# Optimization experiments

Measured on AMD Instinct MI355X. Metric: run time of the kernel, lower is better.

Reference implementation:

```python
import jax, jax.numpy as jnp
import numpy as np

EMBED_DIM = 1024
HEAD_NUM = 16
HEAD_DIM = EMBED_DIM // HEAD_NUM
T, B, S = 2048, 4, 2048


def setup_inputs() -> dict:
    key = jax.random.key(0)
    ks = jax.random.split(key, 11)
    s = 0.02
    return {
        "query": jax.random.normal(ks[0], (T, B, EMBED_DIM), jnp.float32),
        "key": jax.random.normal(ks[1], (S, B, EMBED_DIM), jnp.float32),
        "value": jax.random.normal(ks[2], (S, B, EMBED_DIM), jnp.float32),
        "q_proj_weight": jax.random.normal(ks[3], (EMBED_DIM, EMBED_DIM), jnp.float32) * s,
        "k_proj_weight": jax.random.normal(ks[4], (EMBED_DIM, EMBED_DIM), jnp.float32) * s,
        "v_proj_weight": jax.random.normal(ks[5], (EMBED_DIM, EMBED_DIM), jnp.float32) * s,
        "in_proj_bias": jax.random.normal(ks[6], (3 * EMBED_DIM,), jnp.float32) * s,
        "bias_k": jax.random.normal(ks[7], (1, 1, EMBED_DIM), jnp.float32) * s,
        "bias_v": jax.random.normal(ks[8], (1, 1, EMBED_DIM), jnp.float32) * s,
        "out_proj_weight": jax.random.normal(ks[9], (EMBED_DIM, EMBED_DIM), jnp.float32) * s,
        "out_proj_bias": jax.random.normal(ks[10], (EMBED_DIM,), jnp.float32) * s,
    }


def reference(query, key, value, q_proj_weight, k_proj_weight, v_proj_weight,
              in_proj_bias, bias_k, bias_v, out_proj_weight, out_proj_bias):
    t, b, e = query.shape
    h, hd = HEAD_NUM, HEAD_DIM
    scaling = float(hd) ** -0.5
    # input projections (F.linear: x @ W.T + b)
    q = (query @ q_proj_weight.T + in_proj_bias[:e]) * scaling          # [T,B,E]
    k = key @ k_proj_weight.T + in_proj_bias[e:2 * e]                   # [S,B,E]
    v = value @ v_proj_weight.T + in_proj_bias[2 * e:]                  # [S,B,E]
    # append bias_k / bias_v token along the sequence dim
    k = jnp.concatenate([k, jnp.broadcast_to(bias_k, (1, b, e))], axis=0)  # [S+1,B,E]
    v = jnp.concatenate([v, jnp.broadcast_to(bias_v, (1, b, e))], axis=0)  # [S+1,B,E]
    # split heads: [L, B, E] -> [B*H, L, hd]
    q = q.reshape(t, b * h, hd).transpose(1, 0, 2)
    k = k.reshape(-1, b * h, hd).transpose(1, 0, 2)
    v = v.reshape(-1, b * h, hd).transpose(1, 0, 2)
    # full O(T*S) attention, as in the original bmm->softmax->bmm
    weights = jax.nn.softmax(jnp.einsum('nqd,nkd->nqk', q, k), axis=-1)  # [B*H,T,S+1]
    out = jnp.einsum('nqk,nkd->nqd', weights, v)                         # [B*H,T,hd]
    out = out.transpose(1, 0, 2).reshape(t, b, e)
    out = out @ out_proj_weight.T + out_proj_bias
    avg_weights = weights.sum(axis=1) / h                                # [B*H,S+1]
    return out, avg_weights
```

## Files before the change

### kernel.cpp

```cpp
#include <hip/hip_runtime.h>

#define T_DIM 2048
#define B_DIM 4
#define S_DIM 2048
#define E_DIM 1024
#define H_NUM 16
#define HD    64
#define NH    64
#define SP1   2049
#define SPAD  2112
#define NCHUNK 33
#define NTOKE ((size_t)T_DIM * B_DIM * E_DIM)

typedef short bf16x8 __attribute__((ext_vector_type(8)));
typedef short bf16x4 __attribute__((ext_vector_type(4)));
typedef float f32x4  __attribute__((ext_vector_type(4)));
typedef float f32x16 __attribute__((ext_vector_type(16)));
typedef unsigned int u32;

#define QSCALE 0.18033688011112042f

#if __has_builtin(__builtin_amdgcn_exp2f)
__device__ __forceinline__ float exp2_fast(float x) { return __builtin_amdgcn_exp2f(x); }
#else
__device__ __forceinline__ float exp2_fast(float x) { return __expf(x * 0.6931471805599453f); }
#endif

__device__ __forceinline__ unsigned short f2bf(float x) {
    union { float f; unsigned int u; } v; v.f = x;
    unsigned int r = v.u + 0x7FFFu + ((v.u >> 16) & 1u);
    return (unsigned short)(r >> 16);
}

__device__ __forceinline__ u32 cvtpk_bf16(float lo, float hi) {
    u32 r;
    asm("v_cvt_pk_bf16_f32 %0, %1, %2" : "=v"(r) : "v"(lo), "v"(hi));
    return r;
}
__device__ __forceinline__ void plswap(u32& a, u32& b) {
    asm("v_permlane32_swap_b32 %0, %1" : "+v"(a), "+v"(b));
}

__device__ __forceinline__ void load_lds16(const void* g, void* l) {
    __builtin_amdgcn_global_load_lds(
        (const __attribute__((address_space(1))) unsigned int*)g,
        (__attribute__((address_space(3))) unsigned int*)l, 16, 0, 0);
}

__global__ __launch_bounds__(256)
void cvt_all(const float* __restrict__ q, const float* __restrict__ k,
             const float* __restrict__ v, const float* __restrict__ w0,
             const float* __restrict__ w1, const float* __restrict__ w2,
             const float* __restrict__ w3, short* __restrict__ indst,
             short* __restrict__ wdst, short* __restrict__ k_h,
             short* __restrict__ v_h, const float* __restrict__ bias_k,
             const float* __restrict__ bias_v)
{
    const int y = blockIdx.y;
    if (y < 3) {
        const float* src = (y == 0) ? q : (y == 1) ? k : v;
        short* d = indst + (size_t)y * NTOKE;
        const size_t i = (size_t)blockIdx.x * 256 + threadIdx.x;
        const float4* s = reinterpret_cast<const float4*>(src) + i * 2;
        float4 a = s[0], b = s[1];
        uint4 o;
        o.x = cvtpk_bf16(a.x, a.y); o.y = cvtpk_bf16(a.z, a.w);
        o.z = cvtpk_bf16(b.x, b.y); o.w = cvtpk_bf16(b.z, b.w);
        *(reinterpret_cast<uint4*>(d) + i) = o;
    } else {
        const size_t gi = (size_t)blockIdx.x * 256 + threadIdx.x;
        const size_t per = (size_t)E_DIM * E_DIM / 8;
        if (gi < 4 * per) {
            const int wsel = (int)(gi / per);
            const size_t i = gi % per;
            const float* src = (wsel == 0) ? w0 : (wsel == 1) ? w1 : (wsel == 2) ? w2 : w3;
            short* d = wdst + (size_t)wsel * E_DIM * E_DIM;
            const float4* s = reinterpret_cast<const float4*>(src) + i * 2;
            float4 a = s[0], b = s[1];
            uint4 o;
            o.x = cvtpk_bf16(a.x, a.y); o.y = cvtpk_bf16(a.z, a.w);
            o.z = cvtpk_bf16(b.x, b.y); o.w = cvtpk_bf16(b.z, b.w);
            *(reinterpret_cast<uint4*>(d) + i) = o;
        } else {
            const size_t fi = gi - 4 * per;
            if (fi < (size_t)(SPAD - S_DIM) * NH * HD) {
                const int d   = (int)(fi & 63);
                const int row = (int)((fi >> 6) & 63);
                const int n   = (int)(fi >> 12);
                short bk = 0, bv = 0;
                if (row == 0) {
                    bk = (short)f2bf(bias_k[(n & 15) * HD + d]);
                    bv = (short)f2bf(bias_v[(n & 15) * HD + d]);
                }
                const size_t idx = ((size_t)n * SPAD + S_DIM + row) * HD + d;
                k_h[idx] = bk;
                v_h[idx] = bv;
            }
        }
    }
}

__global__ __launch_bounds__(256, 2)
void gemm_qkv(const short* __restrict__ Abase, const short* __restrict__ Wall,
              const float* __restrict__ biasAll, short* __restrict__ outp)
{
    __shared__ short As[2][128][64];
    __shared__ short Bs[2][128][64];
    const int bm = blockIdx.x, bn = blockIdx.y;
    const int z = blockIdx.z;
    const short* Az = Abase + (size_t)z * NTOKE;
    const short* W  = Wall + (size_t)z * E_DIM * E_DIM;
    const float* bias = biasAll + z * E_DIM;

    const int tid = threadIdx.x;
    const int l = tid & 63, w = tid >> 6;
    const int wr = w >> 1, wc = w & 1;
    const int lr = l & 15, lg = l >> 4;
    const int srow = tid >> 3, scol = (tid & 7) * 8;

    auto stage = [&](int b, int k0) {
#pragma unroll
        for (int r = 0; r < 4; ++r) {
            const int row = r * 32 + srow;
            load_lds16(Az + (size_t)(bm * 128 + row) * E_DIM + k0 + scol, &As[b][row][scol]);
            load_lds16(W + (size_t)(bn * 128 + row) * E_DIM + k0 + scol, &Bs[b][row][scol]);
        }
    };

    stage(0, 0);
    __syncthreads();

    f32x4 acc[4][4] = {};
    int buf = 0;

    for (int k0 = 0; k0 < E_DIM; k0 += 64) {
        if (k0 + 64 < E_DIM) stage(buf ^ 1, k0 + 64);

        __builtin_amdgcn_s_setprio(1);
#pragma unroll
        for (int c = 0; c < 2; ++c) {
            bf16x8 af[4], bf[4];
#pragma unroll
            for (int mi = 0; mi < 4; ++mi)
                af[mi] = *reinterpret_cast<const bf16x8*>(&As[buf][wr * 64 + mi * 16 + lr][c * 32 + lg * 8]);
#pragma unroll
            for (int ni = 0; ni < 4; ++ni)
                bf[ni] = *reinterpret_cast<const bf16x8*>(&Bs[buf][wc * 64 + ni * 16 + lr][c * 32 + lg * 8]);
#pragma unroll
            for (int mi = 0; mi < 4; ++mi)
#pragma unroll
                for (int ni = 0; ni < 4; ++ni)
                    acc[mi][ni] = __builtin_amdgcn_mfma_f32_16x16x32_bf16(
                        af[mi], bf[ni], acc[mi][ni], 0, 0, 0);
        }
        __builtin_amdgcn_s_setprio(0);
        __syncthreads();
        buf ^= 1;
    }

#pragma unroll
    for (int mi = 0; mi < 4; ++mi)
#pragma unroll
        for (int ni = 0; ni < 4; ++ni) {
            const int colg = bn * 128 + wc * 64 + ni * 16 + lr;
            const float bv = bias[colg];
#pragma unroll
            for (int r = 0; r < 4; ++r) {
                const int m = bm * 128 + wr * 64 + mi * 16 + lg * 4 + r;
                float v = acc[mi][ni][r] + bv;
                if (z == 0) v *= QSCALE;
                const int seq = m >> 2, b = m & 3;
                const int head = colg >> 6, d = colg & 63;
                const int sd = (z == 0) ? T_DIM : SPAD;
                short* ob = outp;
                if (z == 1) ob += (size_t)NH * T_DIM * HD;
                else if (z == 2) ob += (size_t)NH * T_DIM * HD + (size_t)NH * SPAD * HD;
                ob[((size_t)(b * 16 + head) * sd + seq) * HD + d] = (short)f2bf(v);
            }
        }
}

__global__ __launch_bounds__(512, 4)
void attn_mfma(const short* __restrict__ q_h, const short* __restrict__ k_h,
               const short* __restrict__ v_h, short* __restrict__ o_h,
               float* __restrict__ m_arr, float* __restrict__ l_arr)
{
    __shared__ short KsD[2][64 * 64];
    __shared__ short VtD[2][64 * 64];

    const int id = blockIdx.x;
    const int xcd = id & 7, slot = id >> 3;
    const int n = xcd * 8 + (slot >> 3);
    const int q0 = (slot & 7) * 256;

    const int tid = threadIdx.x, l = tid & 63, w = tid >> 6;
    const int ql = l & 31;
    const int hi = l >> 5;
    const int qrow = q0 + w * 32 + ql;

    const int krow = tid >> 3, kcg = tid & 7;
    const int kswz = (kcg * 16) ^ ((krow & 7) << 4);
    const int sp = tid & 31, dq = tid >> 5;

    const short* kbase = k_h + (size_t)n * SPAD * HD;
    const short* vbase = v_h + (size_t)n * SPAD * HD;

    bf16x8 aq0, aq1, aq2, aq3;
    {
        const short* qp = q_h + ((size_t)n * T_DIM + qrow) * HD + hi * 8;
        aq0 = *(const bf16x8*)(qp);
        aq1 = *(const bf16x8*)(qp + 16);
        aq2 = *(const bf16x8*)(qp + 32);
        aq3 = *(const bf16x8*)(qp + 48);
    }

    bf16x8 pk  = *(const bf16x8*)(kbase + (size_t)krow * HD + kcg * 8);
    bf16x4 pva = *(const bf16x4*)(vbase + (size_t)(2 * sp) * HD + dq * 4);
    bf16x4 pvb = *(const bf16x4*)(vbase + (size_t)(2 * sp + 1) * HD + dq * 4);
    {
        char* KsB = (char*)KsD[0];
        char* VtB = (char*)VtD[0];
        *(bf16x8*)(KsB + krow * 128 + kswz) = pk;
#pragma unroll
        for (int j = 0; j < 4; ++j) {
            u32 pkd = (u32)(unsigned short)pva[j] | ((u32)(unsigned short)pvb[j] << 16);
            const int d = dq * 4 + j;
            *(u32*)(VtB + d * 128 + ((4 * sp) ^ ((d & 7) << 4))) = pkd;
        }
    }
    __syncthreads();

    float m_run = 0.0f;
    float l_run = 0.0f;
    f32x16 accA, accB;
#pragma unroll
    for (int r = 0; r < 16; ++r) { accA[r] = 0.f; accB[r] = 0.f; }

    for (int kc = 0; kc < NCHUNK; ++kc) {
        const char* KsB = (const char*)KsD[kc & 1];
        const char* VtB = (const char*)VtD[kc & 1];
        const bool more = (kc + 1 < NCHUNK);

        if (more) {
            const int s0n = (kc + 1) * 64;
            pk  = *(const bf16x8*)(kbase + (size_t)(s0n + krow) * HD + kcg * 8);
            pva = *(const bf16x4*)(vbase + (size_t)(s0n + 2 * sp) * HD + dq * 4);
            pvb = *(const bf16x4*)(vbase + (size_t)(s0n + 2 * sp + 1) * HD + dq * 4);
        }

        f32x16 sc0, sc1;
        const float nm = -m_run;
#pragma unroll
        for (int r = 0; r < 16; ++r) { sc0[r] = nm; sc1[r] = nm; }
        __builtin_amdgcn_s_setprio(1);
#pragma unroll
        for (int sl = 0; sl < 4; ++sl) {
            const int cb = ((sl * 32) + hi * 16) ^ ((ql & 7) << 4);
            bf16x8 kf0 = *(const bf16x8*)(KsB + ql * 128 + cb);
            bf16x8 kf1 = *(const bf16x8*)(KsB + (32 + ql) * 128 + cb);
            bf16x8 qf = (sl == 0) ? aq0 : (sl == 1) ? aq1 : (sl == 2) ? aq2 : aq3;
            sc0 = __builtin_amdgcn_mfma_f32_32x32x16_bf16(kf0, qf, sc0, 0, 0, 0);
            sc1 = __builtin_amdgcn_mfma_f32_32x32x16_bf16(kf1, qf, sc1, 0, 0, 0);
        }
        __builtin_amdgcn_s_setprio(0);

        const int s0 = kc * 64;
        if (s0 + 64 > SP1) {
#pragma unroll
            for (int r = 0; r < 16; ++r) {
                const int key = (r & 3) + 8 * (r >> 2) + 4 * hi;
                if (s0 + key >= SP1)      sc0[r] = -1e30f;
                if (s0 + 32 + key >= SP1) sc1[r] = -1e30f;
            }
        }

        float mv[16];
#pragma unroll
        for (int r = 0; r < 16; ++r) mv[r] = fmaxf(sc0[r], sc1[r]);
#pragma unroll
        for (int s = 8; s > 0; s >>= 1)
#pragma unroll
            for (int r = 0; r < s; ++r) mv[r] = fmaxf(mv[r], mv[r + s]);
        const float mx = fmaxf(mv[0], __shfl_xor(mv[0], 32));
        if (!__all(mx <= 8.0f)) {
            const float sh = fmaxf(mx, 0.0f);
            const float fac = exp2_fast(-sh);
            l_run *= fac;
#pragma unroll
            for (int r = 0; r < 16; ++r) {
                accA[r] *= fac; accB[r] *= fac;
                sc0[r] -= sh;   sc1[r] -= sh;
            }
            m_run += sh;
        }
        float p0[16], p1[16];
#pragma unroll
        for (int r = 0; r < 16; ++r) p0[r] = exp2_fast(sc0[r]);
#pragma unroll
        for (int r = 0; r < 16; ++r) p1[r] = exp2_fast(sc1[r]);
        float sv[16];
#pragma unroll
        for (int r = 0; r < 16; ++r) sv[r] = p0[r] + p1[r];
#pragma unroll
        for (int s = 8; s > 0; s >>= 1)
#pragma unroll
            for (int r = 0; r < s; ++r) sv[r] += sv[r + s];
        l_run += sv[0] + __shfl_xor(sv[0], 32);

        union PF { u32 u[4]; bf16x8 v; };
        PF pf0, pf1, pf2, pf3;
        {
            u32 a0 = cvtpk_bf16(p0[0], p0[1]),   b0 = cvtpk_bf16(p0[4], p0[5]);   plswap(a0, b0);
            u32 a1 = cvtpk_bf16(p0[2], p0[3]),   b1 = cvtpk_bf16(p0[6], p0[7]);   plswap(a1, b1);
            u32 a2 = cvtpk_bf16(p0[8], p0[9]),   b2 = cvtpk_bf16(p0[12], p0[13]); plswap(a2, b2);
            u32 a3 = cvtpk_bf16(p0[10], p0[11]), b3 = cvtpk_bf16(p0[14], p0[15]); plswap(a3, b3);
            pf0.u[0] = a0; pf0.u[1] = a1; pf0.u[2] = b0; pf0.u[3] = b1;
            pf1.u[0] = a2; pf1.u[1] = a3; pf1.u[2] = b2; pf1.u[3] = b3;
            u32 c0 = cvtpk_bf16(p1[0], p1[1]),   d0_ = cvtpk_bf16(p1[4], p1[5]);   plswap(c0, d0_);
            u32 c1 = cvtpk_bf16(p1[2], p1[3]),   d1_ = cvtpk_bf16(p1[6], p1[7]);   plswap(c1, d1_);
            u32 c2 = cvtpk_bf16(p1[8], p1[9]),   d2_ = cvtpk_bf16(p1[12], p1[13]); plswap(c2, d2_);
            u32 c3 = cvtpk_bf16(p1[10], p1[11]), d3_ = cvtpk_bf16(p1[14], p1[15]); plswap(c3, d3_);
            pf2.u[0] = c0; pf2.u[1] = c1; pf2.u[2] = d0_; pf2.u[3] = d1_;
            pf3.u[0] = c2; pf3.u[1] = c3; pf3.u[2] = d2_; pf3.u[3] = d3_;
        }

        __builtin_amdgcn_s_setprio(1);
#pragma unroll
        for (int ksl = 0; ksl < 4; ++ksl) {
            const int cb = ((ksl * 32) + hi * 16) ^ ((ql & 7) << 4);
            bf16x8 vf0 = *(const bf16x8*)(VtB + ql * 128 + cb);
            bf16x8 vf1 = *(const bf16x8*)(VtB + (32 + ql) * 128 + cb);
            const bf16x8 pv = (ksl == 0) ? pf0.v : (ksl == 1) ? pf1.v : (ksl == 2) ? pf2.v : pf3.v;
            accA = __builtin_amdgcn_mfma_f32_32x32x16_bf16(vf0, pv, accA, 0, 0, 0);
            accB = __builtin_amdgcn_mfma_f32_32x32x16_bf16(vf1, pv, accB, 0, 0, 0);
        }
        __builtin_amdgcn_s_setprio(0);

        if (more) {
            char* KsN = (char*)KsD[(kc & 1) ^ 1];
            char* VtN = (char*)VtD[(kc & 1) ^ 1];
            *(bf16x8*)(KsN + krow * 128 + kswz) = pk;
#pragma unroll
            for (int j = 0; j < 4; ++j) {
                u32 pkd = (u32)(unsigned short)pva[j] | ((u32)(unsigned short)pvb[j] << 16);
                const int d = dq * 4 + j;
                *(u32*)(VtN + d * 128 + ((4 * sp) ^ ((d & 7) << 4))) = pkd;
            }
            __syncthreads();
        }
    }

    const float il = 1.0f / l_run;
    short* orow = o_h + ((size_t)n * T_DIM + qrow) * HD;
#pragma unroll
    for (int rq = 0; rq < 4; ++rq) {
        uint2 st;
        st.x = cvtpk_bf16(accA[rq * 4 + 0] * il, accA[rq * 4 + 1] * il);
        st.y = cvtpk_bf16(accA[rq * 4 + 2] * il, accA[rq * 4 + 3] * il);
        *(uint2*)(orow + rq * 8 + hi * 4) = st;
        uint2 st2;
        st2.x = cvtpk_bf16(accB[rq * 4 + 0] * il, accB[rq * 4 + 1] * il);
        st2.y = cvtpk_bf16(accB[rq * 4 + 2] * il, accB[rq * 4 + 3] * il);
        *(uint2*)(orow + 32 + rq * 8 + hi * 4) = st2;
    }
    if (hi == 0) {
        m_arr[n * T_DIM + qrow] = m_run;
        l_arr[n * T_DIM + qrow] = l_run;
    }
}

__global__ __launch_bounds__(256)
void tail_fused(const short* __restrict__ q_h, const short* __restrict__ k_h,
                const float* __restrict__ m_arr, const float* __restrict__ l_arr,
                const short* __restrict__ o_h, const short* __restrict__ wob,
                const float* __restrict__ out_b, float* __restrict__ out,
                float* __restrict__ avg_out)
{
    __shared__ char smem[32768];
    const int bid = blockIdx.x;
    const int tid = threadIdx.x;

    if (bid < 2112) {
        short (*Qs)[64][72] = (short(*)[64][72])smem;
        float* msh = (float*)(smem + 18432);
        float* lih = msh + 128;

        const int xcd = bid & 7, slot = bid >> 3;
        const int n = xcd * 8 + slot / 33;
        const int s0 = (slot % 33) * 64;

        const int l = tid & 63, w = tid >> 6;
        const int lr = l & 15, lg = l >> 4;
        const int qr = tid >> 3, qcg = tid & 7;

        const short* qbase = q_h + (size_t)n * T_DIM * HD;

        bf16x8 ak[2];
#pragma unroll
        for (int c = 0; c < 2; ++c)
            ak[c] = *reinterpret_cast<const bf16x8*>(
                k_h + ((size_t)n * SPAD + s0 + w * 16 + lr) * HD + c * 32 + lg * 8);

        bf16x8 qa = *(const bf16x8*)(qbase + (size_t)qr * HD + qcg * 8);
        bf16x8 qb = *(const bf16x8*)(qbase + (size_t)(32 + qr) * HD + qcg * 8);
        float mlv = 0.f;
        if (tid < 64) mlv = m_arr[n * T_DIM + tid];
        else if (tid < 128) mlv = l_arr[n * T_DIM + tid - 64];
        *(bf16x8*)&Qs[0][qr][qcg * 8] = qa;
        *(bf16x8*)&Qs[0][32 + qr][qcg * 8] = qb;
        if (tid < 64) msh[tid] = mlv;
        else if (tid < 128) lih[tid - 64] = 1.0f / mlv;
        __syncthreads();

        float csum[4] = {0.f, 0.f, 0.f, 0.f};

        for (int it = 0; it < T_DIM / 64; ++it) {
            const int buf = it & 1;
            const bool more = (it + 1 < T_DIM / 64);
            if (more) {
                const int qo = (it + 1) * 64;
                qa = *(const bf16x8*)(qbase + (size_t)(qo + qr) * HD + qcg * 8);
                qb = *(const bf16x8*)(qbase + (size_t)(qo + 32 + qr) * HD + qcg * 8);
                if (tid < 64) mlv = m_arr[n * T_DIM + qo + tid];
                else if (tid < 128) mlv = l_arr[n * T_DIM + qo + tid - 64];
            }
            __builtin_amdgcn_s_setprio(1);
#pragma unroll
            for (int qt = 0; qt < 4; ++qt) {
                bf16x8 bq0 = *reinterpret_cast<const bf16x8*>(&Qs[buf][qt * 16 + lr][lg * 8]);
                bf16x8 bq1 = *reinterpret_cast<const bf16x8*>(&Qs[buf][qt * 16 + lr][32 + lg * 8]);
                const float mq = msh[buf * 64 + qt * 16 + lr];
                const float lq = lih[buf * 64 + qt * 16 + lr];
                f32x4 z;
#pragma unroll
                for (int r = 0; r < 4; ++r) z[r] = -mq;
                z = __builtin_amdgcn_mfma_f32_16x16x32_bf16(ak[0], bq0, z, 0, 0, 0);
                z = __builtin_amdgcn_mfma_f32_16x16x32_bf16(ak[1], bq1, z, 0, 0, 0);
#pragma unroll
                for (int r = 0; r < 4; ++r)
                    csum[r] += exp2_fast(z[r]) * lq;
            }
            __builtin_amdgcn_s_setprio(0);
            if (more) {
                *(bf16x8*)&Qs[buf ^ 1][qr][qcg * 8] = qa;
                *(bf16x8*)&Qs[buf ^ 1][32 + qr][qcg * 8] = qb;
                if (tid < 64) msh[(buf ^ 1) * 64 + tid] = mlv;
                else if (tid < 128) lih[(buf ^ 1) * 64 + tid - 64] = 1.0f / mlv;
                __syncthreads();
            }
        }

#pragma unroll
        for (int r = 0; r < 4; ++r) {
            float v = csum[r];
            v += __shfl_xor(v, 1, 16);
            v += __shfl_xor(v, 2, 16);
            v += __shfl_xor(v, 4, 16);
            v += __shfl_xor(v, 8, 16);
            if (lr == 0) {
                const int key = s0 + w * 16 + lg * 4 + r;
                if (key < SP1) avg_out[(size_t)n * SP1 + key] = v * 0.0625f;
            }
        }
    } else {
        short (*As)[64] = (short(*)[64])smem;
        short (*Bs)[64] = (short(*)[64])(smem + 16384);

        const int idx = bid - 2112;
        const int bm = idx & 63, bn = idx >> 6;

        const int l = tid & 63, w = tid >> 6;
        const int wr = w >> 1, wc = w & 1;
        const int lr = l & 15, lg = l >> 4;
        const int srow = tid >> 3, scol = (tid & 7) * 8;

        f32x4 acc[4][4] = {};

        for (int k0 = 0; k0 < E_DIM; k0 += 64) {
#pragma unroll
            for (int r = 0; r < 4; ++r) {
                const int row = r * 32 + srow;
                const int m = bm * 128 + row;
                const short* ga = o_h +
                    ((size_t)((m & 3) * 16 + (k0 >> 6)) * T_DIM + (m >> 2)) * HD + scol;
                load_lds16(ga, &As[row][scol]);
                load_lds16(wob + (size_t)(bn * 128 + row) * E_DIM + k0 + scol, &Bs[row][scol]);
            }
            __syncthreads();

            __builtin_amdgcn_s_setprio(1);
#pragma unroll
            for (int c = 0; c < 2; ++c) {
                bf16x8 af[4], bf[4];
#pragma unroll
                for (int mi = 0; mi < 4; ++mi)
                    af[mi] = *reinterpret_cast<const bf16x8*>(&As[wr * 64 + mi * 16 + lr][c * 32 + lg * 8]);
#pragma unroll
                for (int ni = 0; ni < 4; ++ni)
                    bf[ni] = *reinterpret_cast<const bf16x8*>(&Bs[wc * 64 + ni * 16 + lr][c * 32 + lg * 8]);
#pragma unroll
                for (int mi = 0; mi < 4; ++mi)
#pragma unroll
                    for (int ni = 0; ni < 4; ++ni)
                        acc[mi][ni] = __builtin_amdgcn_mfma_f32_16x16x32_bf16(
                            af[mi], bf[ni], acc[mi][ni], 0, 0, 0);
            }
            __builtin_amdgcn_s_setprio(0);
            __syncthreads();
        }

#pragma unroll
        for (int mi = 0; mi < 4; ++mi)
#pragma unroll
            for (int ni = 0; ni < 4; ++ni) {
                const int colg = bn * 128 + wc * 64 + ni * 16 + lr;
                const float bv = out_b[colg];
#pragma unroll
                for (int r = 0; r < 4; ++r) {
                    const int m = bm * 128 + wr * 64 + mi * 16 + lg * 4 + r;
                    out[(size_t)m * E_DIM + colg] = acc[mi][ni][r] + bv;
                }
            }
    }
}

extern "C" void kernel_launch(void* const* d_in, const int* in_sizes, int n_in,
                              void* d_out, int out_size, void* d_ws, size_t ws_size,
                              hipStream_t stream)
{
    const float* query   = (const float*)d_in[0];
    const float* key     = (const float*)d_in[1];
    const float* value   = (const float*)d_in[2];
    const float* wq      = (const float*)d_in[3];
    const float* wk      = (const float*)d_in[4];
    const float* wv      = (const float*)d_in[5];
    const float* in_bias = (const float*)d_in[6];
    const float* bias_k  = (const float*)d_in[7];
    const float* bias_v  = (const float*)d_in[8];
    const float* wo      = (const float*)d_in[9];
    const float* out_b   = (const float*)d_in[10];
    float* out = (float*)d_out;

    short* wqb    = (short*)d_ws;
    short* wob    = wqb + (size_t)3 * E_DIM * E_DIM;
    short* qkv_bf = wqb + (size_t)4 * E_DIM * E_DIM;
    short* q_h = qkv_bf + 3 * NTOKE;
    short* k_h = q_h + (size_t)NH * T_DIM * HD;
    short* v_h = k_h + (size_t)NH * SPAD * HD;
    short* o_h = v_h + (size_t)NH * SPAD * HD;
    float* m_arr = (float*)(o_h + (size_t)NH * T_DIM * HD);
    float* l_arr = m_arr + (size_t)NH * T_DIM;

    const dim3 blk(256);
    hipLaunchKernelGGL(cvt_all, dim3(4096, 4), blk, 0, stream,
                       query, key, value, wq, wk, wv, wo, qkv_bf, wqb,
                       k_h, v_h, bias_k, bias_v);

    hipLaunchKernelGGL(gemm_qkv, dim3(64, 8, 3), blk, 0, stream,
                       qkv_bf, wqb, in_bias, q_h);
    hipLaunchKernelGGL(attn_mfma, dim3(512), dim3(512), 0, stream,
                       q_h, k_h, v_h, o_h, m_arr, l_arr);
    hipLaunchKernelGGL(tail_fused, dim3(2112 + 512), blk, 0, stream,
                       q_h, k_h, m_arr, l_arr, o_h, wob, out_b,
                       out, out + (size_t)T_DIM * B_DIM * E_DIM);
}
```

Before: 315.2 us.

## Single-buffer QKV GEMM for occupancy, max3 reductions, reorder tail blocks with smaller LDS

The QKV projection GEMM drops its double-buffered LDS staging for a single buffer and raises launch bounds to four blocks per CU, trading load/compute overlap for more resident waves. The attention row-max reduction now uses v_max3_f32 to shorten the reduction chain. In the fused tail kernel, the output-projection GEMM blocks move ahead of the avg-weights blocks, use a 32-wide K step to shrink shared memory, and the m/l arrays are laid out as 2D buffers. Losing the prefetch buffer risks exposed global-load latency in the GEMM.

After: 297.0 us. 5.8% less time.

```diff
diff --git a/kernel.cpp b/kernel.cpp
--- a/kernel.cpp
+++ b/kernel.cpp
@@ -39,6 +39,11 @@
 }
 __device__ __forceinline__ void plswap(u32& a, u32& b) {
     asm("v_permlane32_swap_b32 %0, %1" : "+v"(a), "+v"(b));
+}
+__device__ __forceinline__ float max3f(float a, float b, float c) {
+    float d;
+    asm("v_max3_f32 %0, %1, %2, %3" : "=v"(d) : "v"(a), "v"(b), "v"(c));
+    return d;
 }
 
 __device__ __forceinline__ void load_lds16(const void* g, void* l) {
@@ -100,12 +105,12 @@
     }
 }
 
-__global__ __launch_bounds__(256, 2)
+__global__ __launch_bounds__(256, 4)
 void gemm_qkv(const short* __restrict__ Abase, const short* __restrict__ Wall,
               const float* __restrict__ biasAll, short* __restrict__ outp)
 {
-    __shared__ short As[2][128][64];
-    __shared__ short Bs[2][128][64];
+    __shared__ short As[128][64];
+    __shared__ short Bs[128][64];
     const int bm = blockIdx.x, bn = blockIdx.y;
     const int z = blockIdx.z;
     const short* Az = Abase + (size_t)z * NTOKE;
@@ -118,23 +123,16 @@
     const int lr = l & 15, lg = l >> 4;
     const int srow = tid >> 3, scol = (tid & 7) * 8;
 
-    auto stage = [&](int b, int k0) {
+    f32x4 acc[4][4] = {};
+
+    for (int k0 = 0; k0 < E_DIM; k0 += 64) {
 #pragma unroll
         for (int r = 0; r < 4; ++r) {
             const int row = r * 32 + srow;
-            load_lds16(Az + (size_t)(bm * 128 + row) * E_DIM + k0 + scol, &As[b][row][scol]);
-            load_lds16(W + (size_t)(bn * 128 + row) * E_DIM + k0 + scol, &Bs[b][row][scol]);
-        }
-    };
-
-    stage(0, 0);
-    __syncthreads();
-
-    f32x4 acc[4][4] = {};
-    int buf = 0;
-
-    for (int k0 = 0; k0 < E_DIM; k0 += 64) {
-        if (k0 + 64 < E_DIM) stage(buf ^ 1, k0 + 64);
+            load_lds16(Az + (size_t)(bm * 128 + row) * E_DIM + k0 + scol, &As[row][scol]);
+            load_lds16(W + (size_t)(bn * 128 + row) * E_DIM + k0 + scol, &Bs[row][scol]);
+        }
+        __syncthreads();
 
         __builtin_amdgcn_s_setprio(1);
 #pragma unroll
@@ -142,10 +140,10 @@
             bf16x8 af[4], bf[4];
 #pragma unroll
             for (int mi = 0; mi < 4; ++mi)
-                af[mi] = *reinterpret_cast<const bf16x8*>(&As[buf][wr * 64 + mi * 16 + lr][c * 32 + lg * 8]);
+                af[mi] = *reinterpret_cast<const bf16x8*>(&As[wr * 64 + mi * 16 + lr][c * 32 + lg * 8]);
 #pragma unroll
             for (int ni = 0; ni < 4; ++ni)
-                bf[ni] = *reinterpret_cast<const bf16x8*>(&Bs[buf][wc * 64 + ni * 16 + lr][c * 32 + lg * 8]);
+                bf[ni] = *reinterpret_cast<const bf16x8*>(&Bs[wc * 64 + ni * 16 + lr][c * 32 + lg * 8]);
 #pragma unroll
             for (int mi = 0; mi < 4; ++mi)
 #pragma unroll
@@ -155,7 +153,6 @@
         }
         __builtin_amdgcn_s_setprio(0);
         __syncthreads();
-        buf ^= 1;
     }
 
 #pragma unroll
@@ -274,14 +271,23 @@
             }
         }
 
-        float mv[16];
-#pragma unroll
-        for (int r = 0; r < 16; ++r) mv[r] = fmaxf(sc0[r], sc1[r]);
-#pragma unroll
-        for (int s = 8; s > 0; s >>= 1)
-#pragma unroll
-            for (int r = 0; r < s; ++r) mv[r] = fmaxf(mv[r], mv[r + s]);
-        const float mx = fmaxf(mv[0], __shfl_xor(mv[0], 32));
+        float a0 = max3f(sc0[0],  sc0[1],  sc0[2]);
+        float a1 = max3f(sc0[3],  sc0[4],  sc0[5]);
+        float a2 = max3f(sc0[6],  sc0[7],  sc0[8]);
+        float a3 = max3f(sc0[9],  sc0[10], sc0[11]);
+        float a4 = max3f(sc0[12], sc0[13], sc0[14]);
+        float a5 = max3f(sc0[15], sc1[0],  sc1[1]);
+        float a6 = max3f(sc1[2],  sc1[3],  sc1[4]);
+        float a7 = max3f(sc1[5],  sc1[6],  sc1[7]);
+        float a8 = max3f(sc1[8],  sc1[9],  sc1[10]);
+        float a9 = max3f(sc1[11], sc1[12], sc1[13]);
+        float aA = fmaxf(sc1[14], sc1[15]);
+        float b0 = max3f(a0, a1, a2);
+        float b1 = max3f(a3, a4, a5);
+        float b2 = max3f(a6, a7, a8);
+        float b3 = fmaxf(a9, aA);
+        float mxl = fmaxf(max3f(b0, b1, b2), b3);
+        const float mx = fmaxf(mxl, __shfl_xor(mxl, 32));
         if (!__all(mx <= 8.0f)) {
             const float sh = fmaxf(mx, 0.0f);
             const float fac = exp2_fast(-sh);
@@ -310,18 +316,18 @@
         union PF { u32 u[4]; bf16x8 v; };
         PF pf0, pf1, pf2, pf3;
         {
-            u32 a0 = cvtpk_bf16(p0[0], p0[1]),   b0 = cvtpk_bf16(p0[4], p0[5]);   plswap(a0, b0);
-            u32 a1 = cvtpk_bf16(p0[2], p0[3]),   b1 = cvtpk_bf16(p0[6], p0[7]);   plswap(a1, b1);
-            u32 a2 = cvtpk_bf16(p0[8], p0[9]),   b2 = cvtpk_bf16(p0[12], p0[13]); plswap(a2, b2);
-            u32 a3 = cvtpk_bf16(p0[10], p0[11]), b3 = cvtpk_bf16(p0[14], p0[15]); plswap(a3, b3);
-            pf0.u[0] = a0; pf0.u[1] = a1; pf0.u[2] = b0; pf0.u[3] = b1;
-            pf1.u[0] = a2; pf1.u[1] = a3; pf1.u[2] = b2; pf1.u[3] = b3;
-            u32 c0 = cvtpk_bf16(p1[0], p1[1]),   d0_ = cvtpk_bf16(p1[4], p1[5]);   plswap(c0, d0_);
-            u32 c1 = cvtpk_bf16(p1[2], p1[3]),   d1_ = cvtpk_bf16(p1[6], p1[7]);   plswap(c1, d1_);
-            u32 c2 = cvtpk_bf16(p1[8], p1[9]),   d2_ = cvtpk_bf16(p1[12], p1[13]); plswap(c2, d2_);
-            u32 c3 = cvtpk_bf16(p1[10], p1[11]), d3_ = cvtpk_bf16(p1[14], p1[15]); plswap(c3, d3_);
-            pf2.u[0] = c0; pf2.u[1] = c1; pf2.u[2] = d0_; pf2.u[3] = d1_;
-            pf3.u[0] = c2; pf3.u[1] = c3; pf3.u[2] = d2_; pf3.u[3] = d3_;
+            u32 a0_ = cvtpk_bf16(p0[0], p0[1]),   b0_ = cvtpk_bf16(p0[4], p0[5]);   plswap(a0_, b0_);
+            u32 a1_ = cvtpk_bf16(p0[2], p0[3]),   b1_ = cvtpk_bf16(p0[6], p0[7]);   plswap(a1_, b1_);
+            u32 a2_ = cvtpk_bf16(p0[8], p0[9]),   b2_ = cvtpk_bf16(p0[12], p0[13]); plswap(a2_, b2_);
+            u32 a3_ = cvtpk_bf16(p0[10], p0[11]), b3_ = cvtpk_bf16(p0[14], p0[15]); plswap(a3_, b3_);
+            pf0.u[0] = a0_; pf0.u[1] = a1_; pf0.u[2] = b0_; pf0.u[3] = b1_;
+            pf1.u[0] = a2_; pf1.u[1] = a3_; pf1.u[2] = b2_; pf1.u[3] = b3_;
+            u32 c0_ = cvtpk_bf16(p1[0], p1[1]),   d0_ = cvtpk_bf16(p1[4], p1[5]);   plswap(c0_, d0_);
+            u32 c1_ = cvtpk_bf16(p1[2], p1[3]),   d1_ = cvtpk_bf16(p1[6], p1[7]);   plswap(c1_, d1_);
+            u32 c2_ = cvtpk_bf16(p1[8], p1[9]),   d2_ = cvtpk_bf16(p1[12], p1[13]); plswap(c2_, d2_);
+            u32 c3_ = cvtpk_bf16(p1[10], p1[11]), d3_ = cvtpk_bf16(p1[14], p1[15]); plswap(c3_, d3_);
+            pf2.u[0] = c0_; pf2.u[1] = c1_; pf2.u[2] = d0_; pf2.u[3] = d1_;
+            pf3.u[0] = c2_; pf3.u[1] = c3_; pf3.u[2] = d2_; pf3.u[3] = d3_;
         }
 
         __builtin_amdgcn_s_setprio(1);
@@ -376,16 +382,71 @@
                 const float* __restrict__ out_b, float* __restrict__ out,
                 float* __restrict__ avg_out)
 {
-    __shared__ char smem[32768];
+    __shared__ char smem[20480];
     const int bid = blockIdx.x;
     const int tid = threadIdx.x;
 
-    if (bid < 2112) {
+    if (bid < 512) {
+        short (*As)[32] = (short(*)[32])smem;
+        short (*Bs)[32] = (short(*)[32])(smem + 8192);
+        const int bm = bid & 63, bn = bid >> 6;
+
+        const int l = tid & 63, w = tid >> 6;
+        const int wr = w >> 1, wc = w & 1;
+        const int lr = l & 15, lg = l >> 4;
+
+        f32x4 acc[4][4] = {};
+
+        for (int k0 = 0; k0 < E_DIM; k0 += 32) {
+#pragma unroll
+            for (int s2 = 0; s2 < 2; ++s2) {
+                const int slot = s2 * 256 + tid;
+                const int row = slot >> 2, col = (slot & 3) * 8;
+                const int m = bm * 128 + row;
+                const short* ga = o_h +
+                    ((size_t)((m & 3) * 16 + (k0 >> 6)) * T_DIM + (m >> 2)) * HD + (k0 & 63) + col;
+                load_lds16(ga, &As[row][col]);
+                load_lds16(wob + (size_t)(bn * 128 + row) * E_DIM + k0 + col, &Bs[row][col]);
+            }
+            __syncthreads();
+
+            __builtin_amdgcn_s_setprio(1);
+            bf16x8 af[4], bf[4];
+#pragma unroll
+            for (int mi = 0; mi < 4; ++mi)
+                af[mi] = *reinterpret_cast<const bf16x8*>(&As[wr * 64 + mi * 16 + lr][lg * 8]);
+#pragma unroll
+            for (int ni = 0; ni < 4; ++ni)
+                bf[ni] = *reinterpret_cast<const bf16x8*>(&Bs[wc * 64 + ni * 16 + lr][lg * 8]);
+#pragma unroll
+            for (int mi = 0; mi < 4; ++mi)
+#pragma unroll
+                for (int ni = 0; ni < 4; ++ni)
+                    acc[mi][ni] = __builtin_amdgcn_mfma_f32_16x16x32_bf16(
+                        af[mi], bf[ni], acc[mi][ni], 0, 0, 0);
+            __builtin_amdgcn_s_setprio(0);
+            __syncthreads();
+        }
+
+#pragma unroll
+        for (int mi = 0; mi < 4; ++mi)
+#pragma unroll
+            for (int ni = 0; ni < 4; ++ni) {
+                const int colg = bn * 128 + wc * 64 + ni * 16 + lr;
+                const float bv = out_b[colg];
+#pragma unroll
+                for (int r = 0; r < 4; ++r) {
+                    const int m = bm * 128 + wr * 64 + mi * 16 + lg * 4 + r;
+                    out[(size_t)m * E_DIM + colg] = acc[mi][ni][r] + bv;
+                }
+            }
+    } else {
         short (*Qs)[64][72] = (short(*)[64][72])smem;
-        float* msh = (float*)(smem + 18432);
-        float* lih = msh + 128;
-
-        const int xcd = bid & 7, slot = bid >> 3;
+        float (*msh)[64] = (float(*)[64])(smem + 18432);
+        float (*lih)[64] = (float(*)[64])(smem + 18944);
+
+        const int cid = bid - 512;
+        const int xcd = cid & 7, slot = cid >> 3;
         const int n = xcd * 8 + slot / 33;
         const int s0 = (slot % 33) * 64;
 
@@ -408,8 +469,8 @@
         else if (tid < 128) mlv = l_arr[n * T_DIM + tid - 64];
         *(bf16x8*)&Qs[0][qr][qcg * 8] = qa;
         *(bf16x8*)&Qs[0][32 + qr][qcg * 8] = qb;
-        if (tid < 64) msh[tid] = mlv;
-        else if (tid < 128) lih[tid - 64] = 1.0f / mlv;
+        if (tid < 64) msh[0][tid] = mlv;
+        else if (tid < 128) lih[0][tid - 64] = 1.0f / mlv;
         __syncthreads();
 
         float csum[4] = {0.f, 0.f, 0.f, 0.f};
@@ -429,8 +490,8 @@
             for (int qt = 0; qt < 4; ++qt) {
                 bf16x8 bq0 = *reinterpret_cast<const bf16x8*>(&Qs[buf][qt * 16 + lr][lg * 8]);
                 bf16x8 bq1 = *reinterpret_cast<const bf16x8*>(&Qs[buf][qt * 16 + lr][32 + lg * 8]);
-                const float mq = msh[buf * 64 + qt * 16 + lr];
-                const float lq = lih[buf * 64 + qt * 16 + lr];
+                const float mq = msh[buf][qt * 16 + lr];
+                const float lq = lih[buf][qt * 16 + lr];
                 f32x4 z;
 #pragma unroll
                 for (int r = 0; r < 4; ++r) z[r] = -mq;
@@ -444,8 +505,8 @@
             if (more) {
                 *(bf16x8*)&Qs[buf ^ 1][qr][qcg * 8] = qa;
                 *(bf16x8*)&Qs[buf ^ 1][32 + qr][qcg * 8] = qb;
-                if (tid < 64) msh[(buf ^ 1) * 64 + tid] = mlv;
-                else if (tid < 128) lih[(buf ^ 1) * 64 + tid - 64] = 1.0f / mlv;
+                if (tid < 64) msh[buf ^ 1][tid] = mlv;
+                else if (tid < 128) lih[buf ^ 1][tid - 64] = 1.0f / mlv;
                 __syncthreads();
             }
         }
@@ -462,65 +523,6 @@
                 if (key < SP1) avg_out[(size_t)n * SP1 + key] = v * 0.0625f;
             }
         }
-    } else {
-        short (*As)[64] = (short(*)[64])smem;
-        short (*Bs)[64] = (short(*)[64])(smem + 16384);
-
-        const int idx = bid - 2112;
-        const int bm = idx & 63, bn = idx >> 6;
-
-        const int l = tid & 63, w = tid >> 6;
-        const int wr = w >> 1, wc = w & 1;
-        const int lr = l & 15, lg = l >> 4;
-        const int srow = tid >> 3, scol = (tid & 7) * 8;
-
-        f32x4 acc[4][4] = {};
-
-        for (int k0 = 0; k0 < E_DIM; k0 += 64) {
-#pragma unroll
-            for (int r = 0; r < 4; ++r) {
-                const int row = r * 32 + srow;
-                const int m = bm * 128 + row;
-                const short* ga = o_h +
-                    ((size_t)((m & 3) * 16 + (k0 >> 6)) * T_DIM + (m >> 2)) * HD + scol;
-                load_lds16(ga, &As[row][scol]);
-                load_lds16(wob + (size_t)(bn * 128 + row) * E_DIM + k0 + scol, &Bs[row][scol]);
-            }
-            __syncthreads();
-
-            __builtin_amdgcn_s_setprio(1);
-#pragma unroll
-            for (int c = 0; c < 2; ++c) {
-                bf16x8 af[4], bf[4];
-#pragma unroll
-                for (int mi = 0; mi < 4; ++mi)
-                    af[mi] = *reinterpret_cast<const bf16x8*>(&As[wr * 64 + mi * 16 + lr][c * 32 + lg * 8]);
-#pragma unroll
-                for (int ni = 0; ni < 4; ++ni)
-                    bf[ni] = *reinterpret_cast<const bf16x8*>(&Bs[wc * 64 + ni * 16 + lr][c * 32 + lg * 8]);
-#pragma unroll
-                for (int mi = 0; mi < 4; ++mi)
-#pragma unroll
-                    for (int ni = 0; ni < 4; ++ni)
-                        acc[mi][ni] = __builtin_amdgcn_mfma_f32_16x16x32_bf16(
-                            af[mi], bf[ni], acc[mi][ni], 0, 0, 0);
-            }
-            __builtin_amdgcn_s_setprio(0);
-            __syncthreads();
-        }
-
-#pragma unroll
-        for (int mi = 0; mi < 4; ++mi)
-#pragma unroll
-            for (int ni = 0; ni < 4; ++ni) {
-                const int colg = bn * 128 + wc * 64 + ni * 16 + lr;
-                const float bv = out_b[colg];
-#pragma unroll
-                for (int r = 0; r < 4; ++r) {
-                    const int m = bm * 128 + wr * 64 + mi * 16 + lg * 4 + r;
-                    out[(size_t)m * E_DIM + colg] = acc[mi][ni][r] + bv;
-                }
-            }
     }
 }
 
@@ -560,7 +562,7 @@
                        qkv_bf, wqb, in_bias, q_h);
     hipLaunchKernelGGL(attn_mfma, dim3(512), dim3(512), 0, stream,
                        q_h, k_h, v_h, o_h, m_arr, l_arr);
-    hipLaunchKernelGGL(tail_fused, dim3(2112 + 512), blk, 0, stream,
+    hipLaunchKernelGGL(tail_fused, dim3(512 + 2112), blk, 0, stream,
                        q_h, k_h, m_arr, l_arr, o_h, wob, out_b,
                        out, out + (size_t)T_DIM * B_DIM * E_DIM);
 }
```
